# Kernel optimization log

Measured on AMD Instinct MI355X. Metric: run time of the kernel, lower is better.

## Reference

```python
import jax, jax.numpy as jnp
import numpy as np

WS = 7
NUM_HEADS = 4


def setup_inputs() -> dict:
    key = jax.random.key(0)
    ks = jax.random.split(key, 5)
    C = 128
    return {
        "x": jax.random.normal(ks[0], (8, 222, 222, C), dtype=jnp.float32),
        "qkv_w": jax.random.normal(ks[1], (C, 3 * C), dtype=jnp.float32) * 0.02,
        "qkv_b": jax.random.normal(ks[2], (3 * C,), dtype=jnp.float32) * 0.02,
        "proj_w": jax.random.normal(ks[3], (C, C), dtype=jnp.float32) * 0.02,
        "proj_b": jax.random.normal(ks[4], (C,), dtype=jnp.float32) * 0.02,
    }


def reference(x, qkv_w, qkv_b, proj_w, proj_b):
    B, H, W, C = x.shape
    ws, nh = WS, NUM_HEADS
    hd = C // nh
    scale = hd ** (-0.5)
    pad_h = (ws - H % ws) % ws
    pad_w = (ws - W % ws) % ws
    xp = jnp.pad(x, ((0, 0), (0, pad_h), (0, pad_w), (0, 0)))
    Hp, Wp = H + pad_h, W + pad_w
    # window partition: [B,Hp,Wp,C] -> [nW, ws*ws, C]
    xw = xp.reshape(B, Hp // ws, ws, Wp // ws, ws, C)
    xw = xw.transpose(0, 1, 3, 2, 4, 5).reshape(-1, ws * ws, C)
    # qkv projection
    qkv = xw @ qkv_w + qkv_b  # [nW, 49, 3C]
    qkv = qkv.reshape(-1, ws * ws, 3, nh, hd).transpose(2, 0, 3, 1, 4)
    q, k, v = qkv[0], qkv[1], qkv[2]  # each [nW, nh, 49, hd]
    attn = jax.nn.softmax(jnp.einsum('whqd,whkd->whqk', q, k) * scale, axis=-1)
    out = jnp.einsum('whqk,whkd->whqd', attn, v)  # [nW, nh, 49, hd]
    out = out.transpose(0, 2, 1, 3).reshape(-1, ws * ws, C)
    out = out @ proj_w + proj_b
    # window reverse: [nW, ws*ws, C] -> [B, Hp, Wp, C]
    out = out.reshape(B, Hp // ws, Wp // ws, ws, ws, C)
    out = out.transpose(0, 1, 3, 2, 4, 5).reshape(B, Hp, Wp, C)
    return out[:, :H, :W, :]
```

## Files before the change

### kernel.cpp

```cpp
#include <hip/hip_runtime.h>
#include <stdint.h>

typedef __attribute__((ext_vector_type(8))) short bf16x8;
typedef __attribute__((ext_vector_type(4))) float f32x4;
typedef __attribute__((ext_vector_type(4))) unsigned int u32x4;

#define IMG 222

__device__ __forceinline__ unsigned short f2bf(float f){
  unsigned int u = __float_as_uint(f);
  return (unsigned short)((u + 0x7fffu + ((u >> 16) & 1u)) >> 16);
}

__device__ __forceinline__ unsigned int pk2bf(float lo, float hi){
  unsigned int r;
  asm("v_cvt_pk_bf16_f32 %0, %1, %2" : "=v"(r) : "v"(lo), "v"(hi));
  return r;
}

__device__ __forceinline__ int sw128(int r, int c){ return r*128 + (c ^ ((r & 7) << 3)); }

__device__ __forceinline__ void rebuild_frag(const unsigned int pk[4][2], int src0, int src1,
                                             bool hiSel, bf16x8 out[2]){
  #pragma unroll
  for (int ks = 0; ks < 2; ++ks){
    u32x4 wv;
    #pragma unroll
    for (int jj = 0; jj < 4; ++jj){
      const int src = (jj >> 1) ? src1 : src0;
      unsigned int va = (unsigned int)__shfl((int)pk[2*ks][jj & 1], src);
      unsigned int vb = (unsigned int)__shfl((int)pk[2*ks+1][jj & 1], src);
      wv[jj] = hiSel ? vb : va;
    }
    out[ks] = __builtin_bit_cast(bf16x8, wv);
  }
}

__global__ void prep_weights(const float* __restrict__ qkv_w,
                             const float* __restrict__ proj_w,
                             unsigned short* __restrict__ qwt,
                             unsigned short* __restrict__ pwt){
  int i = blockIdx.x * blockDim.x + threadIdx.x;
  if (i < 384*128){ int n = i >> 7, k = i & 127; qwt[i] = f2bf(qkv_w[k*384 + n]); }
  if (i < 128*128){ int n = i >> 7, k = i & 127; pwt[i] = f2bf(proj_w[k*128 + n]); }
}

__global__ __launch_bounds__(256, 4)
void win_attn(const float* __restrict__ x,
              const float* __restrict__ qkv_b,
              const float* __restrict__ proj_b,
              const unsigned short* __restrict__ qwt,
              const unsigned short* __restrict__ pwt,
              float* __restrict__ out)
{
  extern __shared__ unsigned short lds[];
  unsigned short* r0 = lds;
  unsigned short* r1 = lds + 8192;

  const int tid = threadIdx.x;
  const int wid = tid >> 6;
  const int l   = tid & 63;
  const int l15 = l & 15;
  const int lhi = l >> 4;

  const int src0 = ((l & 16) << 1) + l15;
  const int src1 = src0 + 16;
  const bool hiSel = (l & 32) != 0;

  const int w  = (blockIdx.x & 7) * 1024 + (blockIdx.x >> 3);
  const int b  = w >> 10;
  const int wi = (w >> 5) & 31;
  const int wj = w & 31;

  {
    const int t  = tid >> 2;
    const int cb = (tid & 3) * 32;
    const int r  = t / 7, c = t - r*7;
    const int gh = wi*7 + r, gw = wj*7 + c;
    const bool valid = (t < 49) && (gh < IMG) && (gw < IMG);
    const float* src = x + (((size_t)((size_t)b*IMG + gh))*IMG + gw)*128 + cb;
    #pragma unroll
    for (int i = 0; i < 8; ++i){
      float4 v = valid ? *(const float4*)(src + i*4) : make_float4(0.f,0.f,0.f,0.f);
      uint2 pk; pk.x = pk2bf(v.x, v.y); pk.y = pk2bf(v.z, v.w);
      *(uint2*)(r0 + sw128(t, cb + i*4)) = pk;
    }
  }
  __syncthreads();

  bf16x8 a[4][4];
  #pragma unroll
  for (int mi = 0; mi < 4; ++mi)
    #pragma unroll
    for (int ks = 0; ks < 4; ++ks)
      a[mi][ks] = *(const bf16x8*)(r0 + sw128(mi*16 + l15, ks*32 + lhi*8));
  __syncthreads();

  const float scale = 0.17677669529663687f;

  #pragma unroll
  for (int s = 0; s < 4; ++s){
    const int nt = wid + s*4;
    bf16x8 bfr[4];
    #pragma unroll
    for (int ks = 0; ks < 4; ++ks)
      bfr[ks] = *(const bf16x8*)(qwt + (nt*16 + l15)*128 + ks*32 + lhi*8);
    const float4 bias4 = *(const float4*)(qkv_b + nt*16 + lhi*4);
    __builtin_amdgcn_s_setprio(1);
    #pragma unroll
    for (int mi = 0; mi < 4; ++mi){
      f32x4 acc = {0.f,0.f,0.f,0.f};
      #pragma unroll
      for (int ks = 0; ks < 4; ++ks)
        acc = __builtin_amdgcn_mfma_f32_16x16x32_bf16(bfr[ks], a[mi][ks], acc, 0, 0, 0);
      uint2 pk;
      if (s < 2){
        pk.x = pk2bf((acc[0]+bias4.x)*scale, (acc[1]+bias4.y)*scale);
        pk.y = pk2bf((acc[2]+bias4.z)*scale, (acc[3]+bias4.w)*scale);
        *(uint2*)(r0 + sw128(mi*16 + l15, nt*16 + lhi*4)) = pk;
      } else {
        pk.x = pk2bf(acc[0]+bias4.x, acc[1]+bias4.y);
        pk.y = pk2bf(acc[2]+bias4.z, acc[3]+bias4.w);
        *(uint2*)(r1 + sw128(mi*16 + l15, (nt-8)*16 + lhi*4)) = pk;
      }
    }
    __builtin_amdgcn_s_setprio(0);
  }

  unsigned int pkv0[4][2], pkv1[4][2];
  {
    const int nt0 = 16 + 2*wid;
    bf16x8 bfr[4];
    #pragma unroll
    for (int ks = 0; ks < 4; ++ks)
      bfr[ks] = *(const bf16x8*)(qwt + (nt0*16 + l15)*128 + ks*32 + lhi*8);
    const float bias = qkv_b[nt0*16 + l15];
    __builtin_amdgcn_s_setprio(1);
    #pragma unroll
    for (int mi = 0; mi < 4; ++mi){
      f32x4 acc = {0.f,0.f,0.f,0.f};
      #pragma unroll
      for (int ks = 0; ks < 4; ++ks)
        acc = __builtin_amdgcn_mfma_f32_16x16x32_bf16(a[mi][ks], bfr[ks], acc, 0, 0, 0);
      pkv0[mi][0] = pk2bf(acc[0]+bias, acc[1]+bias);
      pkv0[mi][1] = pk2bf(acc[2]+bias, acc[3]+bias);
    }
    __builtin_amdgcn_s_setprio(0);
  }
  {
    const int nt1 = 17 + 2*wid;
    bf16x8 bfr[4];
    #pragma unroll
    for (int ks = 0; ks < 4; ++ks)
      bfr[ks] = *(const bf16x8*)(qwt + (nt1*16 + l15)*128 + ks*32 + lhi*8);
    const float bias = qkv_b[nt1*16 + l15];
    __builtin_amdgcn_s_setprio(1);
    #pragma unroll
    for (int mi = 0; mi < 4; ++mi){
      f32x4 acc = {0.f,0.f,0.f,0.f};
      #pragma unroll
      for (int ks = 0; ks < 4; ++ks)
        acc = __builtin_amdgcn_mfma_f32_16x16x32_bf16(a[mi][ks], bfr[ks], acc, 0, 0, 0);
      pkv1[mi][0] = pk2bf(acc[0]+bias, acc[1]+bias);
      pkv1[mi][1] = pk2bf(acc[2]+bias, acc[3]+bias);
    }
    __builtin_amdgcn_s_setprio(0);
  }
  __syncthreads();

  const int h = wid;
  bf16x8 aq[4], bk[4];
  #pragma unroll
  for (int i = 0; i < 4; ++i){
    aq[i] = *(const bf16x8*)(r0 + sw128(i*16 + l15, h*32 + lhi*8));
    bk[i] = *(const bf16x8*)(r1 + sw128(i*16 + l15, h*32 + lhi*8));
  }
  __syncthreads();

  bf16x8 pa[4][2];
  float invs[4];
  #pragma unroll
  for (int mi = 0; mi < 4; ++mi){
    f32x4 st[4];
    __builtin_amdgcn_s_setprio(1);
    #pragma unroll
    for (int ni = 0; ni < 4; ++ni){
      f32x4 z = {0.f,0.f,0.f,0.f};
      st[ni] = __builtin_amdgcn_mfma_f32_16x16x32_bf16(bk[ni], aq[mi], z, 0, 0, 0);
    }
    __builtin_amdgcn_s_setprio(0);
    st[3][1] = -1e30f; st[3][2] = -1e30f; st[3][3] = -1e30f;
    if (lhi != 0) st[3][0] = -1e30f;
    float m = st[0][0];
    #pragma unroll
    for (int ni = 0; ni < 4; ++ni)
      #pragma unroll
      for (int r = 0; r < 4; ++r)
        m = fmaxf(m, st[ni][r]);
    m = fmaxf(m, __shfl_xor(m, 16));
    m = fmaxf(m, __shfl_xor(m, 32));
    float e[4][4], s = 0.f;
    #pragma unroll
    for (int ni = 0; ni < 4; ++ni)
      #pragma unroll
      for (int r = 0; r < 4; ++r){
        e[ni][r] = __expf(st[ni][r] - m);
        s += e[ni][r];
      }
    s += __shfl_xor(s, 16);
    s += __shfl_xor(s, 32);
    invs[mi] = __builtin_amdgcn_rcpf(s);
    unsigned int epk[4][2];
    #pragma unroll
    for (int ni = 0; ni < 4; ++ni){
      epk[ni][0] = pk2bf(e[ni][0], e[ni][1]);
      epk[ni][1] = pk2bf(e[ni][2], e[ni][3]);
    }
    rebuild_frag(epk, src0, src1, hiSel, pa[mi]);
  }

  bf16x8 bv0[2], bv1[2];
  rebuild_frag(pkv0, src0, src1, hiSel, bv0);
  rebuild_frag(pkv1, src0, src1, hiSel, bv1);
  #pragma unroll
  for (int mi = 0; mi < 4; ++mi){
    const float is = invs[mi];
    __builtin_amdgcn_s_setprio(1);
    f32x4 acc0 = {0.f,0.f,0.f,0.f}, acc1 = {0.f,0.f,0.f,0.f};
    acc0 = __builtin_amdgcn_mfma_f32_16x16x32_bf16(bv0[0], pa[mi][0], acc0, 0, 0, 0);
    acc0 = __builtin_amdgcn_mfma_f32_16x16x32_bf16(bv0[1], pa[mi][1], acc0, 0, 0, 0);
    acc1 = __builtin_amdgcn_mfma_f32_16x16x32_bf16(bv1[0], pa[mi][0], acc1, 0, 0, 0);
    acc1 = __builtin_amdgcn_mfma_f32_16x16x32_bf16(bv1[1], pa[mi][1], acc1, 0, 0, 0);
    __builtin_amdgcn_s_setprio(0);
    uint2 pk0, pk1;
    pk0.x = pk2bf(acc0[0]*is, acc0[1]*is);
    pk0.y = pk2bf(acc0[2]*is, acc0[3]*is);
    pk1.x = pk2bf(acc1[0]*is, acc1[1]*is);
    pk1.y = pk2bf(acc1[2]*is, acc1[3]*is);
    *(uint2*)(r0 + sw128(mi*16 + l15, h*32 + lhi*4))      = pk0;
    *(uint2*)(r0 + sw128(mi*16 + l15, h*32 + 16 + lhi*4)) = pk1;
  }
  __syncthreads();

  bf16x8 ao[4][4];
  #pragma unroll
  for (int mi = 0; mi < 4; ++mi)
    #pragma unroll
    for (int ks = 0; ks < 4; ++ks)
      ao[mi][ks] = *(const bf16x8*)(r0 + sw128(mi*16 + l15, ks*32 + lhi*8));

  #pragma unroll
  for (int nj = 0; nj < 2; ++nj){
    const int ni = wid + nj*4;
    bf16x8 pbw[4];
    #pragma unroll
    for (int ks = 0; ks < 4; ++ks)
      pbw[ks] = *(const bf16x8*)(pwt + (ni*16 + l15)*128 + ks*32 + lhi*8);
    const float4 bias4 = *(const float4*)(proj_b + ni*16 + lhi*4);
    #pragma unroll
    for (int mi = 0; mi < 4; ++mi){
      __builtin_amdgcn_s_setprio(1);
      f32x4 acc = {0.f,0.f,0.f,0.f};
      #pragma unroll
      for (int ks = 0; ks < 4; ++ks)
        acc = __builtin_amdgcn_mfma_f32_16x16x32_bf16(pbw[ks], ao[mi][ks], acc, 0, 0, 0);
      __builtin_amdgcn_s_setprio(0);
      const int t = mi*16 + l15;
      if (t < 49){
        const int rr = t / 7, cc = t - rr*7;
        const int gh = wi*7 + rr, gw = wj*7 + cc;
        if (gh < IMG && gw < IMG){
          float4 o = make_float4(acc[0]+bias4.x, acc[1]+bias4.y,
                                 acc[2]+bias4.z, acc[3]+bias4.w);
          *(float4*)(out + (((size_t)((size_t)b*IMG + gh))*IMG + gw)*128 + ni*16 + lhi*4) = o;
        }
      }
    }
  }
}

extern "C" void kernel_launch(void* const* d_in, const int* in_sizes, int n_in,
                              void* d_out, int out_size, void* d_ws, size_t ws_size,
                              hipStream_t stream) {
  const float* x      = (const float*)d_in[0];
  const float* qkv_w  = (const float*)d_in[1];
  const float* qkv_b  = (const float*)d_in[2];
  const float* proj_w = (const float*)d_in[3];
  const float* proj_b = (const float*)d_in[4];
  float* out = (float*)d_out;

  unsigned short* qwt = (unsigned short*)d_ws;
  unsigned short* pwt = qwt + 384*128;

  hipLaunchKernelGGL(prep_weights, dim3(192), dim3(256), 0, stream,
                     qkv_w, proj_w, qwt, pwt);
  hipLaunchKernelGGL(win_attn, dim3(8192), dim3(256), 32768, stream,
                     x, qkv_b, proj_b, qwt, pwt, out);
}
```

Baseline: 210.2 us.

## Keep per-head Q/K in registers via shuffles and stage V through LDS

Each wave now computes Q and K for its own head directly and rebuilds the MFMA operand fragments with cross-lane shuffles instead of writing Q/K to LDS and reading them back. This removes two block-wide barriers and the LDS round trip for Q/K. V is instead written per-head into an LDS region with a 64-wide swizzle and read back as fragments, replacing the previous shuffle rebuild of V. This trades LDS traffic and syncs for more shuffle instructions and higher register pressure from holding pkq/pkk.

After: 241.2 us. 1.15x slower.

```diff
diff --git a/kernel.cpp b/kernel.cpp
--- a/kernel.cpp
+++ b/kernel.cpp
@@ -19,6 +19,7 @@
 }
 
 __device__ __forceinline__ int sw128(int r, int c){ return r*128 + (c ^ ((r & 7) << 3)); }
+__device__ __forceinline__ int sw64 (int r, int c){ return r*64  + (c ^ ((r & 7) << 3)); }
 
 __device__ __forceinline__ void rebuild_frag(const unsigned int pk[4][2], int src0, int src1,
                                              bool hiSel, bf16x8 out[2]){
@@ -34,6 +35,19 @@
     }
     out[ks] = __builtin_bit_cast(bf16x8, wv);
   }
+}
+
+__device__ __forceinline__ bf16x8 rebuild_half(const unsigned int p0[2], const unsigned int p1[2],
+                                               int src0, int src1, bool hiSel){
+  u32x4 wv;
+  #pragma unroll
+  for (int jj = 0; jj < 4; ++jj){
+    const int src = (jj >> 1) ? src1 : src0;
+    unsigned int va = (unsigned int)__shfl((int)p0[jj & 1], src);
+    unsigned int vb = (unsigned int)__shfl((int)p1[jj & 1], src);
+    wv[jj] = hiSel ? vb : va;
+  }
+  return __builtin_bit_cast(bf16x8, wv);
 }
 
 __global__ void prep_weights(const float* __restrict__ qkv_w,
@@ -97,85 +111,81 @@
   __syncthreads();
 
   const float scale = 0.17677669529663687f;
-
-  #pragma unroll
-  for (int s = 0; s < 4; ++s){
-    const int nt = wid + s*4;
+  const int h = wid;
+
+  unsigned int pkq[2][4][2], pkk[2][4][2];
+  #pragma unroll
+  for (int t2 = 0; t2 < 2; ++t2){
+    {
+      const int nt = 2*h + t2;
+      bf16x8 bfr[4];
+      #pragma unroll
+      for (int ks = 0; ks < 4; ++ks)
+        bfr[ks] = *(const bf16x8*)(qwt + (nt*16 + l15)*128 + ks*32 + lhi*8);
+      const float4 b4 = *(const float4*)(qkv_b + nt*16 + lhi*4);
+      __builtin_amdgcn_s_setprio(1);
+      #pragma unroll
+      for (int mi = 0; mi < 4; ++mi){
+        f32x4 acc = {0.f,0.f,0.f,0.f};
+        #pragma unroll
+        for (int ks = 0; ks < 4; ++ks)
+          acc = __builtin_amdgcn_mfma_f32_16x16x32_bf16(bfr[ks], a[mi][ks], acc, 0, 0, 0);
+        pkq[t2][mi][0] = pk2bf((acc[0]+b4.x)*scale, (acc[1]+b4.y)*scale);
+        pkq[t2][mi][1] = pk2bf((acc[2]+b4.z)*scale, (acc[3]+b4.w)*scale);
+      }
+      __builtin_amdgcn_s_setprio(0);
+    }
+    {
+      const int nt = 8 + 2*h + t2;
+      bf16x8 bfr[4];
+      #pragma unroll
+      for (int ks = 0; ks < 4; ++ks)
+        bfr[ks] = *(const bf16x8*)(qwt + (nt*16 + l15)*128 + ks*32 + lhi*8);
+      const float4 b4 = *(const float4*)(qkv_b + nt*16 + lhi*4);
+      __builtin_amdgcn_s_setprio(1);
+      #pragma unroll
+      for (int mi = 0; mi < 4; ++mi){
+        f32x4 acc = {0.f,0.f,0.f,0.f};
+        #pragma unroll
+        for (int ks = 0; ks < 4; ++ks)
+          acc = __builtin_amdgcn_mfma_f32_16x16x32_bf16(bfr[ks], a[mi][ks], acc, 0, 0, 0);
+        pkk[t2][mi][0] = pk2bf(acc[0]+b4.x, acc[1]+b4.y);
+        pkk[t2][mi][1] = pk2bf(acc[2]+b4.z, acc[3]+b4.w);
+      }
+      __builtin_amdgcn_s_setprio(0);
+    }
+  }
+  unsigned short* vh = r1 + h*2048;
+  #pragma unroll
+  for (int t2 = 0; t2 < 2; ++t2){
+    const int nt = 16 + 2*h + t2;
     bf16x8 bfr[4];
     #pragma unroll
     for (int ks = 0; ks < 4; ++ks)
       bfr[ks] = *(const bf16x8*)(qwt + (nt*16 + l15)*128 + ks*32 + lhi*8);
-    const float4 bias4 = *(const float4*)(qkv_b + nt*16 + lhi*4);
+    const float bias = qkv_b[nt*16 + l15];
     __builtin_amdgcn_s_setprio(1);
     #pragma unroll
     for (int mi = 0; mi < 4; ++mi){
       f32x4 acc = {0.f,0.f,0.f,0.f};
       #pragma unroll
       for (int ks = 0; ks < 4; ++ks)
-        acc = __builtin_amdgcn_mfma_f32_16x16x32_bf16(bfr[ks], a[mi][ks], acc, 0, 0, 0);
+        acc = __builtin_amdgcn_mfma_f32_16x16x32_bf16(a[mi][ks], bfr[ks], acc, 0, 0, 0);
       uint2 pk;
-      if (s < 2){
-        pk.x = pk2bf((acc[0]+bias4.x)*scale, (acc[1]+bias4.y)*scale);
-        pk.y = pk2bf((acc[2]+bias4.z)*scale, (acc[3]+bias4.w)*scale);
-        *(uint2*)(r0 + sw128(mi*16 + l15, nt*16 + lhi*4)) = pk;
-      } else {
-        pk.x = pk2bf(acc[0]+bias4.x, acc[1]+bias4.y);
-        pk.y = pk2bf(acc[2]+bias4.z, acc[3]+bias4.w);
-        *(uint2*)(r1 + sw128(mi*16 + l15, (nt-8)*16 + lhi*4)) = pk;
-      }
+      pk.x = pk2bf(acc[0]+bias, acc[1]+bias);
+      pk.y = pk2bf(acc[2]+bias, acc[3]+bias);
+      *(uint2*)(vh + sw64(t2*16 + l15, mi*16 + lhi*4)) = pk;
     }
     __builtin_amdgcn_s_setprio(0);
   }
 
-  unsigned int pkv0[4][2], pkv1[4][2];
-  {
-    const int nt0 = 16 + 2*wid;
-    bf16x8 bfr[4];
-    #pragma unroll
-    for (int ks = 0; ks < 4; ++ks)
-      bfr[ks] = *(const bf16x8*)(qwt + (nt0*16 + l15)*128 + ks*32 + lhi*8);
-    const float bias = qkv_b[nt0*16 + l15];
-    __builtin_amdgcn_s_setprio(1);
-    #pragma unroll
-    for (int mi = 0; mi < 4; ++mi){
-      f32x4 acc = {0.f,0.f,0.f,0.f};
-      #pragma unroll
-      for (int ks = 0; ks < 4; ++ks)
-        acc = __builtin_amdgcn_mfma_f32_16x16x32_bf16(a[mi][ks], bfr[ks], acc, 0, 0, 0);
-      pkv0[mi][0] = pk2bf(acc[0]+bias, acc[1]+bias);
-      pkv0[mi][1] = pk2bf(acc[2]+bias, acc[3]+bias);
-    }
-    __builtin_amdgcn_s_setprio(0);
-  }
-  {
-    const int nt1 = 17 + 2*wid;
-    bf16x8 bfr[4];
-    #pragma unroll
-    for (int ks = 0; ks < 4; ++ks)
-      bfr[ks] = *(const bf16x8*)(qwt + (nt1*16 + l15)*128 + ks*32 + lhi*8);
-    const float bias = qkv_b[nt1*16 + l15];
-    __builtin_amdgcn_s_setprio(1);
-    #pragma unroll
-    for (int mi = 0; mi < 4; ++mi){
-      f32x4 acc = {0.f,0.f,0.f,0.f};
-      #pragma unroll
-      for (int ks = 0; ks < 4; ++ks)
-        acc = __builtin_amdgcn_mfma_f32_16x16x32_bf16(a[mi][ks], bfr[ks], acc, 0, 0, 0);
-      pkv1[mi][0] = pk2bf(acc[0]+bias, acc[1]+bias);
-      pkv1[mi][1] = pk2bf(acc[2]+bias, acc[3]+bias);
-    }
-    __builtin_amdgcn_s_setprio(0);
-  }
-  __syncthreads();
-
-  const int h = wid;
   bf16x8 aq[4], bk[4];
   #pragma unroll
-  for (int i = 0; i < 4; ++i){
-    aq[i] = *(const bf16x8*)(r0 + sw128(i*16 + l15, h*32 + lhi*8));
-    bk[i] = *(const bf16x8*)(r1 + sw128(i*16 + l15, h*32 + lhi*8));
-  }
-  __syncthreads();
+  for (int mi = 0; mi < 4; ++mi)
+    aq[mi] = rebuild_half(pkq[0][mi], pkq[1][mi], src0, src1, hiSel);
+  #pragma unroll
+  for (int ni = 0; ni < 4; ++ni)
+    bk[ni] = rebuild_half(pkk[0][ni], pkk[1][ni], src0, src1, hiSel);
 
   bf16x8 pa[4][2];
   float invs[4];
@@ -219,18 +229,21 @@
     rebuild_frag(epk, src0, src1, hiSel, pa[mi]);
   }
 
-  bf16x8 bv0[2], bv1[2];
-  rebuild_frag(pkv0, src0, src1, hiSel, bv0);
-  rebuild_frag(pkv1, src0, src1, hiSel, bv1);
+  bf16x8 bv[2][2];
+  #pragma unroll
+  for (int nc = 0; nc < 2; ++nc)
+    #pragma unroll
+    for (int ks = 0; ks < 2; ++ks)
+      bv[nc][ks] = *(const bf16x8*)(vh + sw64(nc*16 + l15, ks*32 + lhi*8));
   #pragma unroll
   for (int mi = 0; mi < 4; ++mi){
     const float is = invs[mi];
     __builtin_amdgcn_s_setprio(1);
     f32x4 acc0 = {0.f,0.f,0.f,0.f}, acc1 = {0.f,0.f,0.f,0.f};
-    acc0 = __builtin_amdgcn_mfma_f32_16x16x32_bf16(bv0[0], pa[mi][0], acc0, 0, 0, 0);
-    acc0 = __builtin_amdgcn_mfma_f32_16x16x32_bf16(bv0[1], pa[mi][1], acc0, 0, 0, 0);
-    acc1 = __builtin_amdgcn_mfma_f32_16x16x32_bf16(bv1[0], pa[mi][0], acc1, 0, 0, 0);
-    acc1 = __builtin_amdgcn_mfma_f32_16x16x32_bf16(bv1[1], pa[mi][1], acc1, 0, 0, 0);
+    acc0 = __builtin_amdgcn_mfma_f32_16x16x32_bf16(bv[0][0], pa[mi][0], acc0, 0, 0, 0);
+    acc0 = __builtin_amdgcn_mfma_f32_16x16x32_bf16(bv[0][1], pa[mi][1], acc0, 0, 0, 0);
+    acc1 = __builtin_amdgcn_mfma_f32_16x16x32_bf16(bv[1][0], pa[mi][0], acc1, 0, 0, 0);
+    acc1 = __builtin_amdgcn_mfma_f32_16x16x32_bf16(bv[1][1], pa[mi][1], acc1, 0, 0, 0);
     __builtin_amdgcn_s_setprio(0);
     uint2 pk0, pk1;
     pk0.x = pk2bf(acc0[0]*is, acc0[1]*is);
```

## Process four windows per block with register prefetch of next window input

Applied to the files above, without the earlier changes.

Each block now loops over four consecutive windows instead of one, launching a quarter as many blocks. The next window's fp32 input is loaded into registers right after the current tile is staged into LDS, so global load latency overlaps with the QKV, attention and projection compute. This trades grid-level parallelism and extra VGPR pressure (32 floats of prefetch held across the compute) for less block launch overhead and better latency hiding. Occupancy may drop if register use rises.

After: 373.2 us. 77.6% more time.

```diff
diff --git a/kernel.cpp b/kernel.cpp
--- a/kernel.cpp
+++ b/kernel.cpp
@@ -6,6 +6,7 @@
 typedef __attribute__((ext_vector_type(4))) unsigned int u32x4;
 
 #define IMG 222
+#define NWIN 4
 
 __device__ __forceinline__ unsigned short f2bf(float f){
   unsigned int u = __float_as_uint(f);
@@ -67,215 +68,230 @@
   const int src1 = src0 + 16;
   const bool hiSel = (l & 32) != 0;
 
-  const int w  = (blockIdx.x & 7) * 1024 + (blockIdx.x >> 3);
-  const int b  = w >> 10;
-  const int wi = (w >> 5) & 31;
-  const int wj = w & 31;
-
-  {
-    const int t  = tid >> 2;
-    const int cb = (tid & 3) * 32;
-    const int r  = t / 7, c = t - r*7;
-    const int gh = wi*7 + r, gw = wj*7 + c;
+  const int g = (blockIdx.x & 7) * 256 + (blockIdx.x >> 3);
+
+  const int t  = tid >> 2;
+  const int cb = (tid & 3) * 32;
+  const int rr0 = t / 7, cc0 = t - rr0*7;
+
+  float4 px[8];
+  auto issue_stage = [&](int wwin){
+    const int bb = wwin >> 10, wwi = (wwin >> 5) & 31, wwj = wwin & 31;
+    const int gh = wwi*7 + rr0, gw = wwj*7 + cc0;
     const bool valid = (t < 49) && (gh < IMG) && (gw < IMG);
-    const float* src = x + (((size_t)((size_t)b*IMG + gh))*IMG + gw)*128 + cb;
+    const float* src = x + (((size_t)(bb*IMG + gh))*IMG + gw)*128 + cb;
+    #pragma unroll
+    for (int i = 0; i < 8; ++i)
+      px[i] = valid ? *(const float4*)(src + i*4) : make_float4(0.f,0.f,0.f,0.f);
+  };
+
+  issue_stage(g*NWIN);
+
+  const float scale = 0.17677669529663687f;
+  const int h = wid;
+
+  for (int it = 0; it < NWIN; ++it){
+    const int w  = g*NWIN + it;
+    const int b  = w >> 10;
+    const int wi = (w >> 5) & 31;
+    const int wj = w & 31;
+
     #pragma unroll
     for (int i = 0; i < 8; ++i){
-      float4 v = valid ? *(const float4*)(src + i*4) : make_float4(0.f,0.f,0.f,0.f);
-      uint2 pk; pk.x = pk2bf(v.x, v.y); pk.y = pk2bf(v.z, v.w);
+      uint2 pk; pk.x = pk2bf(px[i].x, px[i].y); pk.y = pk2bf(px[i].z, px[i].w);
       *(uint2*)(r0 + sw128(t, cb + i*4)) = pk;
     }
-  }
-  __syncthreads();
-
-  bf16x8 a[4][4];
-  #pragma unroll
-  for (int mi = 0; mi < 4; ++mi)
-    #pragma unroll
-    for (int ks = 0; ks < 4; ++ks)
-      a[mi][ks] = *(const bf16x8*)(r0 + sw128(mi*16 + l15, ks*32 + lhi*8));
-  __syncthreads();
-
-  const float scale = 0.17677669529663687f;
-
-  #pragma unroll
-  for (int s = 0; s < 4; ++s){
-    const int nt = wid + s*4;
-    bf16x8 bfr[4];
-    #pragma unroll
-    for (int ks = 0; ks < 4; ++ks)
-      bfr[ks] = *(const bf16x8*)(qwt + (nt*16 + l15)*128 + ks*32 + lhi*8);
-    const float4 bias4 = *(const float4*)(qkv_b + nt*16 + lhi*4);
-    __builtin_amdgcn_s_setprio(1);
+    __syncthreads();
+
+    bf16x8 a[4][4];
+    #pragma unroll
+    for (int mi = 0; mi < 4; ++mi)
+      #pragma unroll
+      for (int ks = 0; ks < 4; ++ks)
+        a[mi][ks] = *(const bf16x8*)(r0 + sw128(mi*16 + l15, ks*32 + lhi*8));
+    __syncthreads();
+
+    if (it + 1 < NWIN) issue_stage(w + 1);
+
+    #pragma unroll
+    for (int s = 0; s < 4; ++s){
+      const int nt = wid + s*4;
+      bf16x8 bfr[4];
+      #pragma unroll
+      for (int ks = 0; ks < 4; ++ks)
+        bfr[ks] = *(const bf16x8*)(qwt + (nt*16 + l15)*128 + ks*32 + lhi*8);
+      const float4 bias4 = *(const float4*)(qkv_b + nt*16 + lhi*4);
+      __builtin_amdgcn_s_setprio(1);
+      #pragma unroll
+      for (int mi = 0; mi < 4; ++mi){
+        f32x4 acc = {0.f,0.f,0.f,0.f};
+        #pragma unroll
+        for (int ks = 0; ks < 4; ++ks)
+          acc = __builtin_amdgcn_mfma_f32_16x16x32_bf16(bfr[ks], a[mi][ks], acc, 0, 0, 0);
+        uint2 pk;
+        if (s < 2){
+          pk.x = pk2bf((acc[0]+bias4.x)*scale, (acc[1]+bias4.y)*scale);
+          pk.y = pk2bf((acc[2]+bias4.z)*scale, (acc[3]+bias4.w)*scale);
+          *(uint2*)(r0 + sw128(mi*16 + l15, nt*16 + lhi*4)) = pk;
+        } else {
+          pk.x = pk2bf(acc[0]+bias4.x, acc[1]+bias4.y);
+          pk.y = pk2bf(acc[2]+bias4.z, acc[3]+bias4.w);
+          *(uint2*)(r1 + sw128(mi*16 + l15, (nt-8)*16 + lhi*4)) = pk;
+        }
+      }
+      __builtin_amdgcn_s_setprio(0);
+    }
+
+    unsigned int pkv0[4][2], pkv1[4][2];
+    {
+      const int nt0 = 16 + 2*h;
+      bf16x8 bfr[4];
+      #pragma unroll
+      for (int ks = 0; ks < 4; ++ks)
+        bfr[ks] = *(const bf16x8*)(qwt + (nt0*16 + l15)*128 + ks*32 + lhi*8);
+      const float bias = qkv_b[nt0*16 + l15];
+      __builtin_amdgcn_s_setprio(1);
+      #pragma unroll
+      for (int mi = 0; mi < 4; ++mi){
+        f32x4 acc = {0.f,0.f,0.f,0.f};
+        #pragma unroll
+        for (int ks = 0; ks < 4; ++ks)
+          acc = __builtin_amdgcn_mfma_f32_16x16x32_bf16(a[mi][ks], bfr[ks], acc, 0, 0, 0);
+        pkv0[mi][0] = pk2bf(acc[0]+bias, acc[1]+bias);
+        pkv0[mi][1] = pk2bf(acc[2]+bias, acc[3]+bias);
+      }
+      __builtin_amdgcn_s_setprio(0);
+    }
+    {
+      const int nt1 = 17 + 2*h;
+      bf16x8 bfr[4];
+      #pragma unroll
+      for (int ks = 0; ks < 4; ++ks)
+        bfr[ks] = *(const bf16x8*)(qwt + (nt1*16 + l15)*128 + ks*32 + lhi*8);
+      const float bias = qkv_b[nt1*16 + l15];
+      __builtin_amdgcn_s_setprio(1);
+      #pragma unroll
+      for (int mi = 0; mi < 4; ++mi){
+        f32x4 acc = {0.f,0.f,0.f,0.f};
+        #pragma unroll
+        for (int ks = 0; ks < 4; ++ks)
+          acc = __builtin_amdgcn_mfma_f32_16x16x32_bf16(a[mi][ks], bfr[ks], acc, 0, 0, 0);
+        pkv1[mi][0] = pk2bf(acc[0]+bias, acc[1]+bias);
+        pkv1[mi][1] = pk2bf(acc[2]+bias, acc[3]+bias);
+      }
+      __builtin_amdgcn_s_setprio(0);
+    }
+    __syncthreads();
+
+    bf16x8 aq[4], bk[4];
+    #pragma unroll
+    for (int i = 0; i < 4; ++i){
+      aq[i] = *(const bf16x8*)(r0 + sw128(i*16 + l15, h*32 + lhi*8));
+      bk[i] = *(const bf16x8*)(r1 + sw128(i*16 + l15, h*32 + lhi*8));
+    }
+    __syncthreads();
+
+    bf16x8 pa[4][2];
+    float invs[4];
     #pragma unroll
     for (int mi = 0; mi < 4; ++mi){
-      f32x4 acc = {0.f,0.f,0.f,0.f};
-      #pragma unroll
-      for (int ks = 0; ks < 4; ++ks)
-        acc = __builtin_amdgcn_mfma_f32_16x16x32_bf16(bfr[ks], a[mi][ks], acc, 0, 0, 0);
-      uint2 pk;
-      if (s < 2){
-        pk.x = pk2bf((acc[0]+bias4.x)*scale, (acc[1]+bias4.y)*scale);
-        pk.y = pk2bf((acc[2]+bias4.z)*scale, (acc[3]+bias4.w)*scale);
-        *(uint2*)(r0 + sw128(mi*16 + l15, nt*16 + lhi*4)) = pk;
-      } else {
-        pk.x = pk2bf(acc[0]+bias4.x, acc[1]+bias4.y);
-        pk.y = pk2bf(acc[2]+bias4.z, acc[3]+bias4.w);
-        *(uint2*)(r1 + sw128(mi*16 + l15, (nt-8)*16 + lhi*4)) = pk;
-      }
-    }
-    __builtin_amdgcn_s_setprio(0);
-  }
-
-  unsigned int pkv0[4][2], pkv1[4][2];
-  {
-    const int nt0 = 16 + 2*wid;
-    bf16x8 bfr[4];
-    #pragma unroll
-    for (int ks = 0; ks < 4; ++ks)
-      bfr[ks] = *(const bf16x8*)(qwt + (nt0*16 + l15)*128 + ks*32 + lhi*8);
-    const float bias = qkv_b[nt0*16 + l15];
-    __builtin_amdgcn_s_setprio(1);
+      f32x4 st[4];
+      __builtin_amdgcn_s_setprio(1);
+      #pragma unroll
+      for (int ni = 0; ni < 4; ++ni){
+        f32x4 z = {0.f,0.f,0.f,0.f};
+        st[ni] = __builtin_amdgcn_mfma_f32_16x16x32_bf16(bk[ni], aq[mi], z, 0, 0, 0);
+      }
+      __builtin_amdgcn_s_setprio(0);
+      st[3][1] = -1e30f; st[3][2] = -1e30f; st[3][3] = -1e30f;
+      if (lhi != 0) st[3][0] = -1e30f;
+      float m = st[0][0];
+      #pragma unroll
+      for (int ni = 0; ni < 4; ++ni)
+        #pragma unroll
+        for (int r = 0; r < 4; ++r)
+          m = fmaxf(m, st[ni][r]);
+      m = fmaxf(m, __shfl_xor(m, 16));
+      m = fmaxf(m, __shfl_xor(m, 32));
+      float e[4][4], s = 0.f;
+      #pragma unroll
+      for (int ni = 0; ni < 4; ++ni)
+        #pragma unroll
+        for (int r = 0; r < 4; ++r){
+          e[ni][r] = __expf(st[ni][r] - m);
+          s += e[ni][r];
+        }
+      s += __shfl_xor(s, 16);
+      s += __shfl_xor(s, 32);
+      invs[mi] = __builtin_amdgcn_rcpf(s);
+      unsigned int epk[4][2];
+      #pragma unroll
+      for (int ni = 0; ni < 4; ++ni){
+        epk[ni][0] = pk2bf(e[ni][0], e[ni][1]);
+        epk[ni][1] = pk2bf(e[ni][2], e[ni][3]);
+      }
+      rebuild_frag(epk, src0, src1, hiSel, pa[mi]);
+    }
+
+    bf16x8 bv0[2], bv1[2];
+    rebuild_frag(pkv0, src0, src1, hiSel, bv0);
+    rebuild_frag(pkv1, src0, src1, hiSel, bv1);
     #pragma unroll
     for (int mi = 0; mi < 4; ++mi){
-      f32x4 acc = {0.f,0.f,0.f,0.f};
-      #pragma unroll
-      for (int ks = 0; ks < 4; ++ks)
-        acc = __builtin_amdgcn_mfma_f32_16x16x32_bf16(a[mi][ks], bfr[ks], acc, 0, 0, 0);
-      pkv0[mi][0] = pk2bf(acc[0]+bias, acc[1]+bias);
-      pkv0[mi][1] = pk2bf(acc[2]+bias, acc[3]+bias);
-    }
-    __builtin_amdgcn_s_setprio(0);
-  }
-  {
-    const int nt1 = 17 + 2*wid;
-    bf16x8 bfr[4];
-    #pragma unroll
-    for (int ks = 0; ks < 4; ++ks)
-      bfr[ks] = *(const bf16x8*)(qwt + (nt1*16 + l15)*128 + ks*32 + lhi*8);
-    const float bias = qkv_b[nt1*16 + l15];
-    __builtin_amdgcn_s_setprio(1);
-    #pragma unroll
-    for (int mi = 0; mi < 4; ++mi){
-      f32x4 acc = {0.f,0.f,0.f,0.f};
-      #pragma unroll
-      for (int ks = 0; ks < 4; ++ks)
-        acc = __builtin_amdgcn_mfma_f32_16x16x32_bf16(a[mi][ks], bfr[ks], acc, 0, 0, 0);
-      pkv1[mi][0] = pk2bf(acc[0]+bias, acc[1]+bias);
-      pkv1[mi][1] = pk2bf(acc[2]+bias, acc[3]+bias);
-    }
-    __builtin_amdgcn_s_setprio(0);
-  }
-  __syncthreads();
-
-  const int h = wid;
-  bf16x8 aq[4], bk[4];
-  #pragma unroll
-  for (int i = 0; i < 4; ++i){
-    aq[i] = *(const bf16x8*)(r0 + sw128(i*16 + l15, h*32 + lhi*8));
-    bk[i] = *(const bf16x8*)(r1 + sw128(i*16 + l15, h*32 + lhi*8));
-  }
-  __syncthreads();
-
-  bf16x8 pa[4][2];
-  float invs[4];
-  #pragma unroll
-  for (int mi = 0; mi < 4; ++mi){
-    f32x4 st[4];
-    __builtin_amdgcn_s_setprio(1);
-    #pragma unroll
-    for (int ni = 0; ni < 4; ++ni){
-      f32x4 z = {0.f,0.f,0.f,0.f};
-      st[ni] = __builtin_amdgcn_mfma_f32_16x16x32_bf16(bk[ni], aq[mi], z, 0, 0, 0);
-    }
-    __builtin_amdgcn_s_setprio(0);
-    st[3][1] = -1e30f; st[3][2] = -1e30f; st[3][3] = -1e30f;
-    if (lhi != 0) st[3][0] = -1e30f;
-    float m = st[0][0];
-    #pragma unroll
-    for (int ni = 0; ni < 4; ++ni)
-      #pragma unroll
-      for (int r = 0; r < 4; ++r)
-        m = fmaxf(m, st[ni][r]);
-    m = fmaxf(m, __shfl_xor(m, 16));
-    m = fmaxf(m, __shfl_xor(m, 32));
-    float e[4][4], s = 0.f;
-    #pragma unroll
-    for (int ni = 0; ni < 4; ++ni)
-      #pragma unroll
-      for (int r = 0; r < 4; ++r){
-        e[ni][r] = __expf(st[ni][r] - m);
-        s += e[ni][r];
-      }
-    s += __shfl_xor(s, 16);
-    s += __shfl_xor(s, 32);
-    invs[mi] = __builtin_amdgcn_rcpf(s);
-    unsigned int epk[4][2];
-    #pragma unroll
-    for (int ni = 0; ni < 4; ++ni){
-      epk[ni][0] = pk2bf(e[ni][0], e[ni][1]);
-      epk[ni][1] = pk2bf(e[ni][2], e[ni][3]);
-    }
-    rebuild_frag(epk, src0, src1, hiSel, pa[mi]);
-  }
-
-  bf16x8 bv0[2], bv1[2];
-  rebuild_frag(pkv0, src0, src1, hiSel, bv0);
-  rebuild_frag(pkv1, src0, src1, hiSel, bv1);
-  #pragma unroll
-  for (int mi = 0; mi < 4; ++mi){
-    const float is = invs[mi];
-    __builtin_amdgcn_s_setprio(1);
-    f32x4 acc0 = {0.f,0.f,0.f,0.f}, acc1 = {0.f,0.f,0.f,0.f};
-    acc0 = __builtin_amdgcn_mfma_f32_16x16x32_bf16(bv0[0], pa[mi][0], acc0, 0, 0, 0);
-    acc0 = __builtin_amdgcn_mfma_f32_16x16x32_bf16(bv0[1], pa[mi][1], acc0, 0, 0, 0);
-    acc1 = __builtin_amdgcn_mfma_f32_16x16x32_bf16(bv1[0], pa[mi][0], acc1, 0, 0, 0);
-    acc1 = __builtin_amdgcn_mfma_f32_16x16x32_bf16(bv1[1], pa[mi][1], acc1, 0, 0, 0);
-    __builtin_amdgcn_s_setprio(0);
-    uint2 pk0, pk1;
-    pk0.x = pk2bf(acc0[0]*is, acc0[1]*is);
-    pk0.y = pk2bf(acc0[2]*is, acc0[3]*is);
-    pk1.x = pk2bf(acc1[0]*is, acc1[1]*is);
-    pk1.y = pk2bf(acc1[2]*is, acc1[3]*is);
-    *(uint2*)(r0 + sw128(mi*16 + l15, h*32 + lhi*4))      = pk0;
-    *(uint2*)(r0 + sw128(mi*16 + l15, h*32 + 16 + lhi*4)) = pk1;
-  }
-  __syncthreads();
-
-  bf16x8 ao[4][4];
-  #pragma unroll
-  for (int mi = 0; mi < 4; ++mi)
-    #pragma unroll
-    for (int ks = 0; ks < 4; ++ks)
-      ao[mi][ks] = *(const bf16x8*)(r0 + sw128(mi*16 + l15, ks*32 + lhi*8));
-
-  #pragma unroll
-  for (int nj = 0; nj < 2; ++nj){
-    const int ni = wid + nj*4;
-    bf16x8 pbw[4];
-    #pragma unroll
-    for (int ks = 0; ks < 4; ++ks)
-      pbw[ks] = *(const bf16x8*)(pwt + (ni*16 + l15)*128 + ks*32 + lhi*8);
-    const float4 bias4 = *(const float4*)(proj_b + ni*16 + lhi*4);
-    #pragma unroll
-    for (int mi = 0; mi < 4; ++mi){
-      __builtin_amdgcn_s_setprio(1);
-      f32x4 acc = {0.f,0.f,0.f,0.f};
-      #pragma unroll
-      for (int ks = 0; ks < 4; ++ks)
-        acc = __builtin_amdgcn_mfma_f32_16x16x32_bf16(pbw[ks], ao[mi][ks], acc, 0, 0, 0);
-      __builtin_amdgcn_s_setprio(0);
-      const int t = mi*16 + l15;
-      if (t < 49){
-        const int rr = t / 7, cc = t - rr*7;
-        const int gh = wi*7 + rr, gw = wj*7 + cc;
-        if (gh < IMG && gw < IMG){
-          float4 o = make_float4(acc[0]+bias4.x, acc[1]+bias4.y,
-                                 acc[2]+bias4.z, acc[3]+bias4.w);
-          *(float4*)(out + (((size_t)((size_t)b*IMG + gh))*IMG + gw)*128 + ni*16 + lhi*4) = o;
+      const float is = invs[mi];
+      __builtin_amdgcn_s_setprio(1);
+      f32x4 acc0 = {0.f,0.f,0.f,0.f}, acc1 = {0.f,0.f,0.f,0.f};
+      acc0 = __builtin_amdgcn_mfma_f32_16x16x32_bf16(bv0[0], pa[mi][0], acc0, 0, 0, 0);
+      acc0 = __builtin_amdgcn_mfma_f32_16x16x32_bf16(bv0[1], pa[mi][1], acc0, 0, 0, 0);
+      acc1 = __builtin_amdgcn_mfma_f32_16x16x32_bf16(bv1[0], pa[mi][0], acc1, 0, 0, 0);
+      acc1 = __builtin_amdgcn_mfma_f32_16x16x32_bf16(bv1[1], pa[mi][1], acc1, 0, 0, 0);
+      __builtin_amdgcn_s_setprio(0);
+      uint2 pk0, pk1;
+      pk0.x = pk2bf(acc0[0]*is, acc0[1]*is);
+      pk0.y = pk2bf(acc0[2]*is, acc0[3]*is);
+      pk1.x = pk2bf(acc1[0]*is, acc1[1]*is);
+      pk1.y = pk2bf(acc1[2]*is, acc1[3]*is);
+      *(uint2*)(r0 + sw128(mi*16 + l15, h*32 + lhi*4))      = pk0;
+      *(uint2*)(r0 + sw128(mi*16 + l15, h*32 + 16 + lhi*4)) = pk1;
+    }
+    __syncthreads();
+
+    bf16x8 ao[4][4];
+    #pragma unroll
+    for (int mi = 0; mi < 4; ++mi)
+      #pragma unroll
+      for (int ks = 0; ks < 4; ++ks)
+        ao[mi][ks] = *(const bf16x8*)(r0 + sw128(mi*16 + l15, ks*32 + lhi*8));
+
+    #pragma unroll
+    for (int nj = 0; nj < 2; ++nj){
+      const int ni = wid + nj*4;
+      bf16x8 pbw[4];
+      #pragma unroll
+      for (int ks = 0; ks < 4; ++ks)
+        pbw[ks] = *(const bf16x8*)(pwt + (ni*16 + l15)*128 + ks*32 + lhi*8);
+      const float4 bias4 = *(const float4*)(proj_b + ni*16 + lhi*4);
+      #pragma unroll
+      for (int mi = 0; mi < 4; ++mi){
+        __builtin_amdgcn_s_setprio(1);
+        f32x4 acc = {0.f,0.f,0.f,0.f};
+        #pragma unroll
+        for (int ks = 0; ks < 4; ++ks)
+          acc = __builtin_amdgcn_mfma_f32_16x16x32_bf16(pbw[ks], ao[mi][ks], acc, 0, 0, 0);
+        __builtin_amdgcn_s_setprio(0);
+        const int tt = mi*16 + l15;
+        if (tt < 49){
+          const int rr = tt / 7, cc = tt - rr*7;
+          const int gh = wi*7 + rr, gw = wj*7 + cc;
+          if (gh < IMG && gw < IMG){
+            float4 o = make_float4(acc[0]+bias4.x, acc[1]+bias4.y,
+                                   acc[2]+bias4.z, acc[3]+bias4.w);
+            *(float4*)(out + (((size_t)((size_t)b*IMG + gh))*IMG + gw)*128 + ni*16 + lhi*4) = o;
+          }
         }
       }
     }
+    if (it + 1 < NWIN) __syncthreads();
   }
 }
 
@@ -294,6 +310,6 @@
 
   hipLaunchKernelGGL(prep_weights, dim3(192), dim3(256), 0, stream,
                      qkv_w, proj_w, qwt, pwt);
-  hipLaunchKernelGGL(win_attn, dim3(8192), dim3(256), 32768, stream,
+  hipLaunchKernelGGL(win_attn, dim3(2048), dim3(256), 32768, stream,
                      x, qkv_b, proj_b, qwt, pwt, out);
 }
```
